# Kernel optimization log

Hardware: AMD Instinct MI355X
Metric: run time of the kernel (lower is better)

Reference implementation:

```python
import jax, jax.numpy as jnp
import numpy as np

B, C, H, W = 32, 192, 56, 56
HEADS, WS, SHIFT, MLP = 6, 7, 3, 4
HID = C * MLP
EPS = 1e-5


def setup_inputs() -> dict:
    key = jax.random.key(0)
    ks = jax.random.split(key, 12)
    s = 0.02
    return {
        "x": jax.random.normal(ks[0], (B, C, H, W), jnp.float32),
        "ln1_g": jnp.ones((C,), jnp.float32),
        "ln1_b": jnp.zeros((C,), jnp.float32),
        "qkv_w": jax.random.normal(ks[1], (3 * C, C), jnp.float32) * s,
        "qkv_b": jnp.zeros((3 * C,), jnp.float32),
        "proj_w": jax.random.normal(ks[2], (C, C), jnp.float32) * s,
        "proj_b": jnp.zeros((C,), jnp.float32),
        "ln2_g": jnp.ones((C,), jnp.float32),
        "ln2_b": jnp.zeros((C,), jnp.float32),
        "conv1_w": jax.random.normal(ks[3], (HID, C, 3, 3), jnp.float32) * s,
        "conv1_b": jnp.zeros((HID,), jnp.float32),
        "conv2_w": jax.random.normal(ks[4], (C, HID, 3, 3), jnp.float32) * s,
        "conv2_b": jnp.zeros((C,), jnp.float32),
    }


def _layernorm_c(x, g, b):
    # channels-first LayerNorm over C of (B,C,H,W)
    m = jnp.mean(x, axis=1, keepdims=True)
    v = jnp.mean((x - m) ** 2, axis=1, keepdims=True)
    return (x - m) * jax.lax.rsqrt(v + EPS) * g[None, :, None, None] + b[None, :, None, None]


def _conv(x, w, b):
    y = jax.lax.conv_general_dilated(x, w, (1, 1), 'SAME',
                                     dimension_numbers=('NCHW', 'OIHW', 'NCHW'))
    return y + b[None, :, None, None]


def _swin_block(x, ln1_g, ln1_b, qkv_w, qkv_b, proj_w, proj_b,
                ln2_g, ln2_b, conv1_w, conv1_b, conv2_w, conv2_b):
    Bx, Cx, Hx, Wx = x.shape
    shortcut = x
    xn = _layernorm_c(x, ln1_g, ln1_b)
    if SHIFT > 0:
        xn = jnp.roll(xn, shift=(-SHIFT, -SHIFT), axis=(2, 3))
    Hp = ((Hx + WS - 1) // WS) * WS
    Wp = ((Wx + WS - 1) // WS) * WS
    if Hp > Hx or Wp > Wx:
        xn = jnp.pad(xn, ((0, 0), (0, 0), (0, Hp - Hx), (0, Wp - Wx)))
    nh, nw = Hp // WS, Wp // WS
    # partition into windows: (B*nh*nw, WS*WS, C)
    xw = xn.reshape(Bx, Cx, nh, WS, nw, WS).transpose(0, 2, 4, 3, 5, 1)
    xw = xw.reshape(Bx * nh * nw, WS * WS, Cx)
    # window MHA
    d = Cx // HEADS
    qkv = xw @ qkv_w.T + qkv_b                     # (B_, N, 3C)
    q, k, v = jnp.split(qkv, 3, axis=-1)
    def heads(t):
        return t.reshape(t.shape[0], t.shape[1], HEADS, d).transpose(0, 2, 1, 3)
    q, k, v = heads(q), heads(k), heads(v)         # (B_, H, N, d)
    attn = jnp.einsum('bhnd,bhmd->bhnm', q, k) * (d ** -0.5)
    attn = jax.nn.softmax(attn, axis=-1)
    out = jnp.einsum('bhnm,bhmd->bhnd', attn, v)
    out = out.transpose(0, 2, 1, 3).reshape(xw.shape[0], WS * WS, Cx)
    out = out @ proj_w.T + proj_b
    # merge windows back
    y = out.reshape(Bx, nh, nw, WS, WS, Cx).transpose(0, 5, 1, 3, 2, 4)
    y = y.reshape(Bx, Cx, Hp, Wp)
    if SHIFT > 0:
        y = jnp.roll(y, shift=(SHIFT, SHIFT), axis=(2, 3))
    y = y[:, :, :Hx, :Wx]
    x = shortcut + y
    h = _layernorm_c(x, ln2_g, ln2_b)
    h = _conv(h, conv1_w, conv1_b)
    h = jax.nn.gelu(h, approximate=False)
    h = _conv(h, conv2_w, conv2_b)
    return x + h


def reference(x, ln1_g, ln1_b, qkv_w, qkv_b, proj_w, proj_b,
              ln2_g, ln2_b, conv1_w, conv1_b, conv2_w, conv2_b):
    return _swin_block(x, ln1_g, ln1_b, qkv_w, qkv_b, proj_w, proj_b,
                       ln2_g, ln2_b, conv1_w, conv1_b, conv2_w, conv2_b)
```

## Files before the change

kernel.cpp:

```cpp
#include <hip/hip_runtime.h>

typedef __bf16 bf16;
typedef __bf16 bf16x8 __attribute__((ext_vector_type(8)));
typedef __bf16 bf16x4 __attribute__((ext_vector_type(4)));
typedef float  f32x4  __attribute__((ext_vector_type(4)));


__device__ __forceinline__ f32x4 mfma16(bf16x8 a, bf16x8 b, f32x4 c) {
    return __builtin_amdgcn_mfma_f32_16x16x32_bf16(a, b, c, 0, 0, 0);
}
__device__ __forceinline__ float ld_in(const void* p, long i, int f32) {
    return f32 ? ((const float*)p)[i] : (float)(((const bf16*)p)[i]);
}
__device__ __forceinline__ void gload16(const bf16* g, bf16* l) {
    __builtin_amdgcn_global_load_lds(
        (const __attribute__((address_space(1))) void*)g,
        (__attribute__((address_space(3))) void*)l, 16, 0, 0);
}

__global__ void k_flag(const unsigned* __restrict__ g, int* __restrict__ flag, unsigned* __restrict__ zp) {
    if (threadIdx.x == 0) *flag = (*g == 0x3F800000u) ? 1 : 0;
    if (threadIdx.x < 32) zp[threadIdx.x] = 0u;
}

__global__ __launch_bounds__(256) void k_prep(const void* __restrict__ c1w, const void* __restrict__ c2w,
                                              bf16* __restrict__ Wt1, bf16* __restrict__ Wt2,
                                              const int* __restrict__ flagp) {
    int f32 = *flagp;
    int i = blockIdx.x * 256 + threadIdx.x;
    int t = i / 147456;
    int r = i - t * 147456;
    { int o = r / 192, c = r - (r / 192) * 192;
      Wt1[i] = (bf16)ld_in(c1w, (long)(o * 192 + c) * 9 + t, f32); }
    { int o = r / 768, c = r - (r / 768) * 768;
      Wt2[i] = (bf16)ld_in(c2w, (long)(o * 768 + c) * 9 + t, f32); }
}

__global__ __launch_bounds__(256) void k_prepw(const void* __restrict__ qkvw, const void* __restrict__ projw,
                                               bf16* __restrict__ Wq, bf16* __restrict__ Wp,
                                               const int* __restrict__ flagp) {
    int f32 = *flagp;
    int i = blockIdx.x * 256 + threadIdx.x;
    if (i < 110592) Wq[i] = (bf16)ld_in(qkvw, i, f32);
    else            Wp[i - 110592] = (bf16)ld_in(projw, (long)i - 110592, f32);
}

__global__ __launch_bounds__(256) void k_ln1(const void* __restrict__ x, const void* __restrict__ g,
                                             const void* __restrict__ be, bf16* __restrict__ xw,
                                             const int* __restrict__ flagp) {
    int f32 = *flagp;
    int m = blockIdx.x * 256 + threadIdx.x;
    int b = m / 3136;
    int r = m - b * 3136;
    int h = r / 56;
    int w = r - h * 56;
    int hs = h + 3; if (hs >= 56) hs -= 56;
    int ws = w + 3; if (ws >= 56) ws -= 56;
    long base = (long)b * 602112 + hs * 56 + ws;
    float s = 0.f, sq = 0.f;
    for (int c = 0; c < 192; c++) { float v = ld_in(x, base + (long)c * 3136, f32); s += v; sq += v * v; }
    float mean = s * (1.f / 192.f);
    float var  = sq * (1.f / 192.f) - mean * mean;
    float rstd = rsqrtf(var + 1e-5f);
    int win = b * 64 + (h / 7) * 8 + (w / 7);
    int tok = (h % 7) * 7 + (w % 7);
    bf16* pd = xw + ((size_t)win * 49 + tok) * 192;
    for (int c = 0; c < 192; c++) {
        float v = ld_in(x, base + (long)c * 3136, f32);
        pd[c] = (bf16)(((v - mean) * rstd) * ld_in(g, c, f32) + ld_in(be, c, f32));
    }
}

__global__ __launch_bounds__(512) void k_attn3(const bf16* __restrict__ xw, const bf16* __restrict__ Wq,
                                               const void* __restrict__ qkvb, bf16* __restrict__ ctx,
                                               const int* __restrict__ flagp) {
    __shared__ __align__(16) bf16 Xs[49 * 200];
    __shared__ __align__(16) bf16 Qs[49 * 72];
    __shared__ __align__(16) bf16 Ks[49 * 72];
    __shared__ __align__(16) bf16 Vt[64 * 72];
    __shared__ __align__(16) bf16 Ps[2 * 49 * 72];
    int f32 = *flagp;
    int win = blockIdx.x;
    int tid = threadIdx.x;
    int wv = tid >> 6, lane = tid & 63, l15 = lane & 15, quad = lane >> 4;
    int wg = wv >> 2, wr = wv & 3;

    {
        const uint4* src = (const uint4*)(xw + (size_t)win * 9408);
        for (int i = tid; i < 1176; i += 512) {
            int row = i / 24, col = i - row * 24;
            *(uint4*)(Xs + row * 200 + col * 8) = src[i];
        }
    }
    __syncthreads();

    int arow = wr * 16 + l15; if (arow > 48) arow = 48;

    for (int pair = 0; pair < 3; pair++) {
        f32x4 acc[6] = {};
        #pragma unroll
        for (int kc = 0; kc < 6; kc++) {
            bf16x8 a = *(const bf16x8*)(Xs + arow * 200 + kc * 32 + quad * 8);
            #pragma unroll
            for (int j = 0; j < 6; j++) {
                int c = wg * 96 + j * 16;
                int part = c >> 6, within = c & 63;
                bf16x8 bb = *(const bf16x8*)(Wq + (size_t)(part * 192 + pair * 64 + within + l15) * 192 + kc * 32 + quad * 8);
                acc[j] = mfma16(a, bb, acc[j]);
            }
        }
        #pragma unroll
        for (int j = 0; j < 6; j++) {
            int c = wg * 96 + j * 16 + l15;
            int part = c >> 6, within = c & 63;
            float bs = ld_in(qkvb, part * 192 + pair * 64 + within, f32);
            #pragma unroll
            for (int rr = 0; rr < 4; rr++) {
                int row = wr * 16 + quad * 4 + rr;
                float v = acc[j][rr] + bs;
                if (part == 0)      { if (row < 49) Qs[row * 72 + within] = (bf16)v; }
                else if (part == 1) { if (row < 49) Ks[row * 72 + within] = (bf16)v; }
                else                Vt[within * 72 + row] = (bf16)v;
            }
        }
        __syncthreads();

        int hoff = wg * 32;
        f32x4 s[4] = {};
        {
            bf16x8 qa = *(const bf16x8*)(Qs + arow * 72 + hoff + quad * 8);
            #pragma unroll
            for (int j = 0; j < 4; j++) {
                int krow = j * 16 + l15; if (krow > 48) krow = 48;
                bf16x8 kb = *(const bf16x8*)(Ks + krow * 72 + hoff + quad * 8);
                s[j] = mfma16(qa, kb, s[j]);
            }
        }
        bf16* Pg = Ps + wg * 49 * 72;
        #pragma unroll
        for (int rr = 0; rr < 4; rr++) {
            float sv[4]; float mx = -1e30f;
            #pragma unroll
            for (int j = 0; j < 4; j++) {
                int c = j * 16 + l15;
                float v = (c <= 48) ? s[j][rr] * 0.17677669529663687f : -1e30f;
                sv[j] = v; mx = fmaxf(mx, v);
            }
            mx = fmaxf(mx, __shfl_xor(mx, 1)); mx = fmaxf(mx, __shfl_xor(mx, 2));
            mx = fmaxf(mx, __shfl_xor(mx, 4)); mx = fmaxf(mx, __shfl_xor(mx, 8));
            float e[4]; float sum = 0.f;
            #pragma unroll
            for (int j = 0; j < 4; j++) { e[j] = __expf(sv[j] - mx); sum += e[j]; }
            sum += __shfl_xor(sum, 1); sum += __shfl_xor(sum, 2);
            sum += __shfl_xor(sum, 4); sum += __shfl_xor(sum, 8);
            float inv = 1.f / sum;
            int row = wr * 16 + quad * 4 + rr;
            if (row < 49) {
                #pragma unroll
                for (int j = 0; j < 4; j++) Pg[row * 72 + j * 16 + l15] = (bf16)(e[j] * inv);
            }
        }
        f32x4 o[2] = {};
        #pragma unroll
        for (int kc = 0; kc < 2; kc++) {
            bf16x8 pa = *(const bf16x8*)(Pg + arow * 72 + kc * 32 + quad * 8);
            #pragma unroll
            for (int j = 0; j < 2; j++) {
                bf16x8 vb = *(const bf16x8*)(Vt + (hoff + j * 16 + l15) * 72 + kc * 32 + quad * 8);
                o[j] = mfma16(pa, vb, o[j]);
            }
        }
        #pragma unroll
        for (int j = 0; j < 2; j++) {
            int d = j * 16 + l15;
            #pragma unroll
            for (int rr = 0; rr < 4; rr++) {
                int tok = wr * 16 + quad * 4 + rr;
                if (tok < 49)
                    ctx[((size_t)win * 49 + tok) * 192 + (pair * 2 + wg) * 32 + d] = (bf16)o[j][rr];
            }
        }
        __syncthreads();
    }
}

__global__ __launch_bounds__(256) void k_proj(const bf16* __restrict__ ctx, const bf16* __restrict__ Wp,
                                              const void* __restrict__ pb, const void* __restrict__ x,
                                              bf16* __restrict__ x2, const int* __restrict__ flagp) {
    __shared__ __align__(16) bf16 As[64 * 200];
    int f32 = *flagp;
    int m0 = blockIdx.x * 64, n0 = blockIdx.y * 64;
    int tid = threadIdx.x;
    {
        int row = tid >> 2, seg = tid & 3;
        const uint4* src = (const uint4*)(ctx + (size_t)(m0 + row) * 192);
        uint4* dst = (uint4*)(As + row * 200);
        #pragma unroll
        for (int p = 0; p < 6; p++) dst[seg + p * 4] = src[seg + p * 4];
    }
    __syncthreads();
    int wv = tid >> 6, lane = tid & 63, l15 = lane & 15, quad = lane >> 4;
    f32x4 acc[4] = {};
    #pragma unroll
    for (int kc = 0; kc < 6; kc++) {
        bf16x8 a = *(const bf16x8*)(As + (wv * 16 + l15) * 200 + kc * 32 + quad * 8);
        #pragma unroll
        for (int j = 0; j < 4; j++) {
            bf16x8 bb = *(const bf16x8*)(Wp + (size_t)(n0 + j * 16 + l15) * 192 + kc * 32 + quad * 8);
            acc[j] = mfma16(a, bb, acc[j]);
        }
    }
    #pragma unroll
    for (int j = 0; j < 4; j++) {
        int n = n0 + j * 16 + l15;
        float bs = ld_in(pb, n, f32);
        #pragma unroll
        for (int rr = 0; rr < 4; rr++) {
            int mrow = m0 + wv * 16 + quad * 4 + rr;
            int win = mrow / 49, tok = mrow - win * 49;
            int b = win >> 6, wr = win & 63;
            int wh = wr >> 3, ww = wr & 7;
            int ty = tok / 7, tx = tok - ty * 7;
            int h = wh * 7 + ty, w = ww * 7 + tx;
            int h0 = h + 3; if (h0 >= 56) h0 -= 56;
            int w0 = w + 3; if (w0 >= 56) w0 -= 56;
            long addr = (long)b * 602112 + (long)n * 3136 + h0 * 56 + w0;
            x2[addr] = (bf16)(acc[j][rr] + bs + ld_in(x, addr, f32));
        }
    }
}

__global__ __launch_bounds__(256) void k_ln2(const bf16* __restrict__ x2, const void* __restrict__ g,
                                             const void* __restrict__ be, bf16* __restrict__ hout,
                                             const int* __restrict__ flagp) {
    int f32 = *flagp;
    int m = blockIdx.x * 256 + threadIdx.x;
    int b = m / 3136;
    int sp = m - b * 3136;
    const bf16* px = x2 + (size_t)b * 602112 + sp;
    float s = 0.f, sq = 0.f;
    for (int c = 0; c < 192; c++) { float v = (float)px[(size_t)c * 3136]; s += v; sq += v * v; }
    float mean = s * (1.f / 192.f);
    float var  = sq * (1.f / 192.f) - mean * mean;
    float rstd = rsqrtf(var + 1e-5f);
    bf16* pd = hout + (size_t)m * 192;
    for (int c = 0; c < 192; c++) {
        float v = (float)px[(size_t)c * 3136];
        pd[c] = (bf16)(((v - mean) * rstd) * ld_in(g, c, f32) + ld_in(be, c, f32));
    }
}

template <int CIN, int COUT, int TN, bool DOGELU, bool RES>
__global__ __launch_bounds__(256) void k_conv(const bf16* __restrict__ in, const bf16* __restrict__ Wt,
                                              const void* __restrict__ bias, const bf16* __restrict__ res,
                                              void* __restrict__ outv, const int* __restrict__ flagp,
                                              const bf16* __restrict__ zp,
                                              int mbase, int in_local, int out_local) {
    constexpr int JW = TN / 32;
    constexpr int BIT = TN / 32;
    __shared__ __align__(16) bf16 As[128 * 64];
    __shared__ __align__(16) bf16 Bs[TN * 64];
    int f32 = *flagp;
    int n0, m0;
    {
        int lin = blockIdx.y * gridDim.x + blockIdx.x;
        int nwg = gridDim.x * gridDim.y;
        int q = nwg >> 3, r = nwg & 7;
        int xcd = lin & 7, idx = lin >> 3;
        int wgid = (xcd < r ? xcd * (q + 1) : r * (q + 1) + (xcd - r) * q) + idx;
        n0 = (wgid % gridDim.x) * TN;
        m0 = mbase + (wgid / gridDim.x) * 128;
    }
    int tid = threadIdx.x;
    int wv = tid >> 6, lane = tid & 63, l15 = lane & 15, quad = lane >> 4;
    int rsub = lane >> 3, c8 = lane & 7;
    int pbv[4], prv[4], qrv[4];
    #pragma unroll
    for (int it = 0; it < 4; it++) {
        int m = m0 + it * 32 + wv * 8 + rsub;
        int b = m / 3136; int sp = m - b * 3136;
        int p = sp / 56;  int q = sp - p * 56;
        pbv[it] = b * 3136 + p * 56 + q - (in_local ? mbase : 0);
        prv[it] = p; qrv[it] = q;
    }
    int wm = wv >> 1, wn = wv & 1;
    f32x4 acc[4][JW] = {};

    for (int t = 0; t < 9; t++) {
        int dy = t / 3 - 1, dx = t - (t / 3) * 3 - 1;
        int doff = dy * 56 + dx;
        for (int kk = 0; kk < CIN; kk += 64) {
            #pragma unroll
            for (int it = 0; it < 4; it++) {
                int pp = prv[it] + dy, qq = qrv[it] + dx;
                bool valid = ((unsigned)pp < 56u) && ((unsigned)qq < 56u);
                const bf16* gsrc = valid ? in + (size_t)(pbv[it] + doff) * CIN + kk + c8 * 8
                                         : zp + c8 * 8;
                gload16(gsrc, As + (it * 32 + wv * 8) * 64);
            }
            #pragma unroll
            for (int it = 0; it < BIT; it++) {
                int brow = it * 32 + wv * 8 + rsub;
                gload16(Wt + ((size_t)t * COUT + n0 + brow) * CIN + kk + c8 * 8,
                        Bs + (it * 32 + wv * 8) * 64);
            }
            __syncthreads();
            #pragma unroll
            for (int kc = 0; kc < 2; kc++) {
                bf16x8 a[4];
                #pragma unroll
                for (int mi = 0; mi < 4; mi++)
                    a[mi] = *(const bf16x8*)(As + (wm * 64 + mi * 16 + l15) * 64 + kc * 32 + quad * 8);
                #pragma unroll
                for (int j = 0; j < JW; j++) {
                    bf16x8 bfr = *(const bf16x8*)(Bs + (wn * (TN / 2) + j * 16 + l15) * 64 + kc * 32 + quad * 8);
                    #pragma unroll
                    for (int mi = 0; mi < 4; mi++) acc[mi][j] = mfma16(a[mi], bfr, acc[mi][j]);
                }
            }
            __syncthreads();
        }
    }
    #pragma unroll
    for (int j = 0; j < JW; j++) {
        int n = n0 + wn * (TN / 2) + j * 16 + l15;
        float bs = ld_in(bias, n, f32);
        #pragma unroll
        for (int mi = 0; mi < 4; mi++) {
            int mgb = m0 + wm * 64 + mi * 16 + quad * 4;
            if (RES) {
                int b = mgb / 3136; int sp = mgb - b * 3136;
                long addr = (long)b * 602112 + (long)n * 3136 + sp;
                bf16x4 r4 = *(const bf16x4*)(res + addr);
                if (f32) {
                    float4 o4;
                    o4.x = acc[mi][j][0] + bs + (float)r4[0];
                    o4.y = acc[mi][j][1] + bs + (float)r4[1];
                    o4.z = acc[mi][j][2] + bs + (float)r4[2];
                    o4.w = acc[mi][j][3] + bs + (float)r4[3];
                    *(float4*)((float*)outv + addr) = o4;
                } else {
                    bf16x4 o4;
                    #pragma unroll
                    for (int rr = 0; rr < 4; rr++) o4[rr] = (bf16)(acc[mi][j][rr] + bs + (float)r4[rr]);
                    *(bf16x4*)((bf16*)outv + addr) = o4;
                }
            } else {
                #pragma unroll
                for (int rr = 0; rr < 4; rr++) {
                    float val = acc[mi][j][rr] + bs;
                    if (DOGELU) val = 0.5f * val * (1.f + erff(val * 0.70710678118654752f));
                    ((bf16*)outv)[(size_t)(mgb + rr - (out_local ? mbase : 0)) * COUT + n] = (bf16)val;
                }
            }
        }
    }
}

extern "C" void kernel_launch(void* const* d_in, const int* in_sizes, int n_in,
                              void* d_out, int out_size, void* d_ws, size_t ws_size,
                              hipStream_t stream) {
    (void)in_sizes; (void)n_in; (void)out_size;
    const void* x     = d_in[0];
    const void* ln1g  = d_in[1];
    const void* ln1b  = d_in[2];
    const void* qkvw  = d_in[3];
    const void* qkvb  = d_in[4];
    const void* projw = d_in[5];
    const void* projb = d_in[6];
    const void* ln2g  = d_in[7];
    const void* ln2b  = d_in[8];
    const void* c1w   = d_in[9];
    const void* c1b   = d_in[10];
    const void* c2w   = d_in[11];
    const void* c2b   = d_in[12];

    char* w = (char*)d_ws;
    int*      flag = (int*)w;
    unsigned* zp   = (unsigned*)(w + 128);
    w += 256;
    bf16* Wt1  = (bf16*)w;  w += 2654208;
    bf16* Wt2  = (bf16*)w;  w += 2654208;
    bf16* bufA = (bf16*)w;  w += 38535168;
    bf16* bufB = (bf16*)w;  w += 38535168;
    char* rest = w;
    bf16* Wq   = (bf16*)rest;
    bf16* Wp   = Wq + 110592;
    bf16* slab = (bf16*)rest;

    size_t fixed = (size_t)(rest - (char*)d_ws);
    size_t avail = ws_size > fixed ? ws_size - fixed : 0;
    int sliceB;
    if      (avail >= (size_t)32 * 3136 * 768 * 2) sliceB = 32;
    else if (avail >= (size_t)16 * 3136 * 768 * 2) sliceB = 16;
    else if (avail >= (size_t)8  * 3136 * 768 * 2) sliceB = 8;
    else                                           sliceB = 4;
    int nsl = 32 / sliceB;
    int slab_px = sliceB * 3136;

    k_flag<<<1, 64, 0, stream>>>((const unsigned*)ln1g, flag, zp);
    k_prep<<<5184, 256, 0, stream>>>(c1w, c2w, Wt1, Wt2, flag);
    k_prepw<<<576, 256, 0, stream>>>(qkvw, projw, Wq, Wp, flag);
    k_ln1<<<392, 256, 0, stream>>>(x, ln1g, ln1b, bufA, flag);
    k_attn3<<<2048, 512, 0, stream>>>(bufA, Wq, qkvb, bufB, flag);
    k_proj<<<dim3(1568, 3), 256, 0, stream>>>(bufB, Wp, projb, x, bufA, flag);
    k_ln2<<<392, 256, 0, stream>>>(bufA, ln2g, ln2b, bufB, flag);
    for (int s = 0; s < nsl; s++) {
        int mbase = s * slab_px;
        k_conv<192, 768, 128, true,  false><<<dim3(6, slab_px / 128), 256, 0, stream>>>(
            bufB, Wt1, c1b, nullptr, (void*)slab, flag, (const bf16*)zp, mbase, 0, 1);
        k_conv<768, 192, 192, false, true ><<<dim3(1, slab_px / 128), 256, 0, stream>>>(
            slab, Wt2, c2b, bufA, d_out, flag, (const bf16*)zp, mbase, 1, 0);
    }
}
```

Before: 1.712 ms.

## Restructure window attention QKV staging and use polynomial GELU approximation

```diff
diff --git a/kernel.cpp b/kernel.cpp
--- a/kernel.cpp
+++ b/kernel.cpp
@@ -16,6 +16,15 @@
     __builtin_amdgcn_global_load_lds(
         (const __attribute__((address_space(1))) void*)g,
         (__attribute__((address_space(3))) void*)l, 16, 0, 0);
+}
+__device__ __forceinline__ float fast_gelu(float x) {
+    float a = fabsf(x) * 0.70710678118654752f;
+    float t = __builtin_amdgcn_rcpf(1.f + 0.3275911f * a);
+    float poly = ((((1.061405429f * t - 1.453152027f) * t + 1.421413741f) * t
+                   - 0.284496736f) * t + 0.254829592f) * t;
+    float er = 1.f - poly * __expf(-a * a);
+    er = copysignf(er, x);
+    return 0.5f * x * (1.f + er);
 }
 
 __global__ void k_flag(const unsigned* __restrict__ g, int* __restrict__ flag, unsigned* __restrict__ zp) {
@@ -71,68 +80,67 @@
     }
 }
 
-__global__ __launch_bounds__(512) void k_attn3(const bf16* __restrict__ xw, const bf16* __restrict__ Wq,
-                                               const void* __restrict__ qkvb, bf16* __restrict__ ctx,
-                                               const int* __restrict__ flagp) {
-    __shared__ __align__(16) bf16 Xs[49 * 200];
-    __shared__ __align__(16) bf16 Qs[49 * 72];
-    __shared__ __align__(16) bf16 Ks[49 * 72];
-    __shared__ __align__(16) bf16 Vt[64 * 72];
+__global__ __launch_bounds__(512, 4) void k_attn3(const bf16* __restrict__ xw, const bf16* __restrict__ Wq,
+                                                  const void* __restrict__ qkvb, bf16* __restrict__ ctx,
+                                                  const int* __restrict__ flagp) {
+    __shared__ __align__(16) bf16 Qs[49 * 200];
+    __shared__ __align__(16) bf16 Ks[49 * 200];
+    __shared__ __align__(16) bf16 Vt[2][64 * 72];
     __shared__ __align__(16) bf16 Ps[2 * 49 * 72];
     int f32 = *flagp;
     int win = blockIdx.x;
     int tid = threadIdx.x;
     int wv = tid >> 6, lane = tid & 63, l15 = lane & 15, quad = lane >> 4;
     int wg = wv >> 2, wr = wv & 3;
-
-    {
-        const uint4* src = (const uint4*)(xw + (size_t)win * 9408);
-        for (int i = tid; i < 1176; i += 512) {
-            int row = i / 24, col = i - row * 24;
-            *(uint4*)(Xs + row * 200 + col * 8) = src[i];
-        }
-    }
-    __syncthreads();
-
     int arow = wr * 16 + l15; if (arow > 48) arow = 48;
-
-    for (int pair = 0; pair < 3; pair++) {
+    const bf16* xsrc = xw + (size_t)win * 9408;
+
+    bf16x4 vrh[2][4];
+
+    #pragma unroll
+    for (int p = 0; p < 3; p++) {
         f32x4 acc[6] = {};
         #pragma unroll
         for (int kc = 0; kc < 6; kc++) {
-            bf16x8 a = *(const bf16x8*)(Xs + arow * 200 + kc * 32 + quad * 8);
+            bf16x8 a = *(const bf16x8*)(xsrc + arow * 192 + kc * 32 + quad * 8);
             #pragma unroll
             for (int j = 0; j < 6; j++) {
                 int c = wg * 96 + j * 16;
                 int part = c >> 6, within = c & 63;
-                bf16x8 bb = *(const bf16x8*)(Wq + (size_t)(part * 192 + pair * 64 + within + l15) * 192 + kc * 32 + quad * 8);
+                bf16x8 bb = *(const bf16x8*)(Wq + (size_t)(part * 192 + p * 64 + within + l15) * 192 + kc * 32 + quad * 8);
                 acc[j] = mfma16(a, bb, acc[j]);
             }
         }
         #pragma unroll
         for (int j = 0; j < 6; j++) {
-            int c = wg * 96 + j * 16 + l15;
-            int part = c >> 6, within = c & 63;
-            float bs = ld_in(qkvb, part * 192 + pair * 64 + within, f32);
+            int c = wg * 96 + j * 16;
+            int part = c >> 6, wcol = (c & 63) + l15;
+            float bs = ld_in(qkvb, part * 192 + p * 64 + wcol, f32);
             #pragma unroll
             for (int rr = 0; rr < 4; rr++) {
                 int row = wr * 16 + quad * 4 + rr;
                 float v = acc[j][rr] + bs;
-                if (part == 0)      { if (row < 49) Qs[row * 72 + within] = (bf16)v; }
-                else if (part == 1) { if (row < 49) Ks[row * 72 + within] = (bf16)v; }
-                else                Vt[within * 72 + row] = (bf16)v;
-            }
-        }
-        __syncthreads();
-
-        int hoff = wg * 32;
+                if (part == 0)      { if (row < 49) Qs[row * 200 + p * 64 + wcol] = (bf16)v; }
+                else if (part == 1) { if (row < 49) Ks[row * 200 + p * 64 + wcol] = (bf16)v; }
+                else {
+                    if (p == 0) Vt[0][wcol * 72 + row] = (bf16)v;
+                    else        vrh[p - 1][j - 2][rr] = (bf16)v;
+                }
+            }
+        }
+    }
+    __syncthreads();
+
+    #pragma unroll
+    for (int p = 0; p < 3; p++) {
+        int hcol = p * 64 + wg * 32;
         f32x4 s[4] = {};
         {
-            bf16x8 qa = *(const bf16x8*)(Qs + arow * 72 + hoff + quad * 8);
+            bf16x8 qa = *(const bf16x8*)(Qs + arow * 200 + hcol + quad * 8);
             #pragma unroll
             for (int j = 0; j < 4; j++) {
                 int krow = j * 16 + l15; if (krow > 48) krow = 48;
-                bf16x8 kb = *(const bf16x8*)(Ks + krow * 72 + hoff + quad * 8);
+                bf16x8 kb = *(const bf16x8*)(Ks + krow * 200 + hcol + quad * 8);
                 s[j] = mfma16(qa, kb, s[j]);
             }
         }
@@ -161,12 +169,13 @@
             }
         }
         f32x4 o[2] = {};
+        const bf16* Vb = Vt[p & 1];
         #pragma unroll
         for (int kc = 0; kc < 2; kc++) {
             bf16x8 pa = *(const bf16x8*)(Pg + arow * 72 + kc * 32 + quad * 8);
             #pragma unroll
             for (int j = 0; j < 2; j++) {
-                bf16x8 vb = *(const bf16x8*)(Vt + (hoff + j * 16 + l15) * 72 + kc * 32 + quad * 8);
+                bf16x8 vb = *(const bf16x8*)(Vb + (wg * 32 + j * 16 + l15) * 72 + kc * 32 + quad * 8);
                 o[j] = mfma16(pa, vb, o[j]);
             }
         }
@@ -177,10 +186,22 @@
             for (int rr = 0; rr < 4; rr++) {
                 int tok = wr * 16 + quad * 4 + rr;
                 if (tok < 49)
-                    ctx[((size_t)win * 49 + tok) * 192 + (pair * 2 + wg) * 32 + d] = (bf16)o[j][rr];
-            }
-        }
-        __syncthreads();
+                    ctx[((size_t)win * 49 + tok) * 192 + (p * 2 + wg) * 32 + d] = (bf16)o[j][rr];
+            }
+        }
+        if (p < 2) {
+            if (wg == 1) {
+                #pragma unroll
+                for (int j2 = 0; j2 < 4; j2++) {
+                    #pragma unroll
+                    for (int rr = 0; rr < 4; rr++) {
+                        int row = wr * 16 + quad * 4 + rr;
+                        Vt[(p + 1) & 1][(j2 * 16 + l15) * 72 + row] = vrh[p][j2][rr];
+                    }
+                }
+            }
+            __syncthreads();
+        }
     }
 }
 
@@ -349,7 +370,7 @@
                 #pragma unroll
                 for (int rr = 0; rr < 4; rr++) {
                     float val = acc[mi][j][rr] + bs;
-                    if (DOGELU) val = 0.5f * val * (1.f + erff(val * 0.70710678118654752f));
+                    if (DOGELU) val = fast_gelu(val);
                     ((bf16*)outv)[(size_t)(mgb + rr - (out_local ? mbase : 0)) * COUT + n] = (bf16)val;
                 }
             }
```

Measured after the change: 1.662 ms. 1.03x faster.
